# Kernel tuning notes

Measured on AMD Instinct MI355X. Metric: run time of the kernel, lower is better.

The kernel has to match this reference:

```python
import jax, jax.numpy as jnp
import numpy as np

N_P, N_D, N_S = 100000, 1000, 5000      # patients, drugs, diseases
C, H, L = 64, 4, 2                       # hidden, heads, layers
DH = C // H                              # head dim
IN_P, IN_D, IN_S = 64, 128, 64           # raw feature dims per node type
E_PD, E_DP, E_DS, E_PS = 300000, 300000, 100000, 100000
EPS = 1e-16


def setup_inputs() -> dict:
    key = jax.random.key(0)
    ks = jax.random.split(key, 20)

    def lin(k, fin, fout, prefix=()):
        return jax.random.normal(k, prefix + (fin, fout), jnp.float32) / np.sqrt(fin).astype(np.float32)

    def edges(k, e, n_src, n_dst):
        k1, k2 = jax.random.split(k)
        return jnp.stack([jax.random.randint(k1, (e,), 0, n_src),
                          jax.random.randint(k2, (e,), 0, n_dst)]).astype(jnp.int32)

    inp = {}
    inp['x_p'] = jax.random.normal(ks[0], (N_P, IN_P), jnp.float32)
    inp['x_d'] = jax.random.normal(ks[1], (N_D, IN_D), jnp.float32)
    inp['x_s'] = jax.random.normal(ks[2], (N_S, IN_S), jnp.float32)
    inp['Win_p'] = lin(ks[3], IN_P, C); inp['bin_p'] = jnp.zeros((C,), jnp.float32)
    inp['Win_d'] = lin(ks[4], IN_D, C); inp['bin_d'] = jnp.zeros((C,), jnp.float32)
    inp['Win_s'] = lin(ks[5], IN_S, C); inp['bin_s'] = jnp.zeros((C,), jnp.float32)
    inp['Wk'] = lin(ks[6], C, C, (L, 3)); inp['bk'] = jnp.zeros((L, 3, C), jnp.float32)
    inp['Wq'] = lin(ks[7], C, C, (L, 3)); inp['bq'] = jnp.zeros((L, 3, C), jnp.float32)
    inp['Wv'] = lin(ks[8], C, C, (L, 3)); inp['bv'] = jnp.zeros((L, 3, C), jnp.float32)
    inp['Wa'] = lin(ks[9], C, C, (L, 3)); inp['ba'] = jnp.zeros((L, 3, C), jnp.float32)
    inp['a_rel'] = jax.random.normal(ks[10], (L, 4, H, DH, DH), jnp.float32) / np.sqrt(DH).astype(np.float32)
    inp['m_rel'] = jax.random.normal(ks[11], (L, 4, H, DH, DH), jnp.float32) / np.sqrt(DH).astype(np.float32)
    inp['p_rel'] = jnp.ones((L, 4, H), jnp.float32)   # PyG inits rel prior to ones
    inp['skip'] = jnp.ones((L, 3), jnp.float32)       # PyG inits skip gate to ones
    inp['ei_pd'] = edges(ks[12], E_PD, N_P, N_D)  # patient -takes-> drug
    inp['ei_dp'] = edges(ks[13], E_DP, N_D, N_P)  # drug -taken_by-> patient
    inp['ei_ds'] = edges(ks[14], E_DS, N_D, N_S)  # drug -treats-> disease
    inp['ei_ps'] = edges(ks[15], E_PS, N_P, N_S)  # patient -has-> disease
    return inp


def _hgt(x_p, x_d, x_s, Win_p, bin_p, Win_d, bin_d, Win_s, bin_s,
         Wk, bk, Wq, bq, Wv, bv, Wa, ba, a_rel, m_rel, p_rel, skip,
         ei_pd, ei_dp, ei_ds, ei_ps):
    Ns = (N_P, N_D, N_S)
    # per-node-type input projection (lin_dict)
    xs = [x_p @ Win_p + bin_p, x_d @ Win_d + bin_d, x_s @ Win_s + bin_s]
    # (src_type, dst_type, edge_index) for each relation
    edge_defs = [(0, 1, ei_pd), (1, 0, ei_dp), (1, 2, ei_ds), (0, 2, ei_ps)]
    inv_sqrt_d = np.float32(1.0 / np.sqrt(DH))

    for l in range(L):  # HGTConv layers
        k_t = [(xs[t] @ Wk[l, t] + bk[l, t]).reshape(Ns[t], H, DH) for t in range(3)]
        q_t = [(xs[t] @ Wq[l, t] + bq[l, t]).reshape(Ns[t], H, DH) for t in range(3)]
        v_t = [(xs[t] @ Wv[l, t] + bv[l, t]).reshape(Ns[t], H, DH) for t in range(3)]
        out = [jnp.zeros((Ns[t], H, DH), xs[t].dtype) for t in range(3)]
        for r, (st, dt, ei) in enumerate(edge_defs):
            src, dst = ei[0], ei[1]
            # relation-specific head-wise transforms of K and V
            k_rel = jnp.einsum('nhd,hde->nhe', k_t[st], a_rel[l, r])
            v_rel = jnp.einsum('nhd,hde->nhe', v_t[st], m_rel[l, r])
            # attention logits per edge, per head: [E, H]
            alpha = (q_t[dt][dst] * k_rel[src]).sum(-1) * (p_rel[l, r] * inv_sqrt_d)
            # segment softmax over incoming edges of each dst node (per relation)
            mx = jax.ops.segment_max(alpha, dst, num_segments=Ns[dt])
            a = jnp.exp(alpha - jax.lax.stop_gradient(mx)[dst])
            den = jax.ops.segment_sum(a, dst, num_segments=Ns[dt])
            a = a / (den[dst] + EPS)
            # attention-weighted scatter-add of messages, grouped by 'sum'
            out[dt] = out[dt] + jax.ops.segment_sum(v_rel[src] * a[:, :, None], dst, num_segments=Ns[dt])
        new_xs = []
        for t in range(3):
            o = jax.nn.gelu(out[t].reshape(Ns[t], C), approximate=False) @ Wa[l, t] + ba[l, t]
            s = jax.nn.sigmoid(skip[l, t])  # learned skip gate (in == out channels)
            new_xs.append(s * o + (1.0 - s) * xs[t])
        xs = new_xs
    # concatenate node-type outputs along node axis: [N_P+N_D+N_S, C]
    return jnp.concatenate(xs, axis=0)


def reference(x_p, x_d, x_s, Win_p, bin_p, Win_d, bin_d, Win_s, bin_s,
              Wk, bk, Wq, bq, Wv, bv, Wa, ba, a_rel, m_rel, p_rel, skip,
              ei_pd, ei_dp, ei_ds, ei_ps):
    return _hgt(x_p, x_d, x_s, Win_p, bin_p, Win_d, bin_d, Win_s, bin_s,
                Wk, bk, Wq, bq, Wv, bv, Wa, ba, a_rel, m_rel, p_rel, skip,
                ei_pd, ei_dp, ei_ds, ei_ps)
```

## Files before the change

### kernel.cpp

```cpp
#include <hip/hip_runtime.h>
#include <cmath>

typedef unsigned short ush;
typedef __attribute__((ext_vector_type(8))) short short8;
typedef __attribute__((ext_vector_type(4))) float floatx4;

static constexpr int N_P = 100000, N_D = 1000, N_S = 5000, NT = N_P + N_D + N_S;
static constexpr int NC = 111000;
static constexpr int E_TOT = 800000;

static constexpr int NB0 = 128, NB2 = 64, NB3 = 64;
static constexpr int CH0 = (300000 + NB0 - 1) / NB0;
static constexpr int CH2 = (100000 + NB2 - 1) / NB2;
static constexpr int HB0_OFF = 0;
static constexpr int HB2_OFF = NB0 * 1000;
static constexpr int HB3_OFF = HB2_OFF + NB2 * 5000;
static constexpr int NCH0 = NB0 / 16, NCH2 = NB2 / 16;
static constexpr int CS0_OFF = 0;
static constexpr int CS2_OFF = NCH0 * 1000;
static constexpr int CS3_OFF = CS2_OFF + NCH2 * 5000;
static constexpr int NHIST = NB0 + NB2 + NB3;
static constexpr int NBLK_R1 = (300000 + 255) / 256;
static constexpr int NZB = (100000 + 255) / 256;

__device__ __forceinline__ float b2f(ush b) { return __uint_as_float(((unsigned)b) << 16); }
__device__ __forceinline__ ush f2b(float f) {
    unsigned u = __float_as_uint(f);
    return (ush)((u + 0x7FFFu + ((u >> 16) & 1u)) >> 16);
}

static constexpr size_t OFF_WINP = 0;
static constexpr size_t OFF_BINP = 4096;
static constexpr size_t OFF_WIND = 4160;
static constexpr size_t OFF_BIND = 12352;
static constexpr size_t OFF_WINS = 12416;
static constexpr size_t OFF_BINS = 16512;
static constexpr size_t OFF_WK = 16576;
static constexpr size_t OFF_BK = 41152;
static constexpr size_t OFF_WQ = 41536;
static constexpr size_t OFF_BQ = 66112;
static constexpr size_t OFF_WV = 66496;
static constexpr size_t OFF_BV = 91072;
static constexpr size_t OFF_WA = 91456;
static constexpr size_t OFF_BA = 116032;
static constexpr size_t OFF_AREL = 116416;
static constexpr size_t OFF_MREL = 124608;
static constexpr size_t OFF_PREL = 132800;
static constexpr size_t OFF_SKIP = 132832;
static constexpr size_t CW_TOTAL = 132838;
static constexpr int NCONVB = (int)((CW_TOTAL + 255) / 256);
static constexpr int NSCB = (NC + 1 + 255) / 256;

static constexpr size_t TWINP = 0;
static constexpr size_t TWIND = 4096;
static constexpr size_t TWINS = 12288;
static constexpr size_t TWQO = 16384;
static constexpr size_t TWAO = 40960;
static constexpr size_t TW_TOTAL = 65536;
static constexpr int NTWB = (int)(TW_TOTAL / 256);

struct ConvArgs {
    const void* src[18];
    long cum[19];
    int fl[18];
};

struct CsrB {
    const int* ei[3];
    const int* ei1;
};

__device__ __forceinline__ void hist_geom(int b, const CsrB& c, int& r, const int*& ei, int& E,
                                          int& ndst, int& e0, int& e1, int& hb) {
    if (b < NB0) {
        r = 0; ei = c.ei[0]; E = 300000; ndst = 1000;
        e0 = b * CH0; hb = HB0_OFF + b * 1000;
    } else if (b < NB0 + NB2) {
        r = 1; ei = c.ei[1]; E = 100000; ndst = 5000;
        e0 = (b - NB0) * CH2; hb = HB2_OFF + (b - NB0) * 5000;
    } else {
        r = 2; ei = c.ei[2]; E = 100000; ndst = 5000;
        e0 = (b - NB0 - NB2) * CH2; hb = HB3_OFF + (b - NB0 - NB2) * 5000;
    }
    e1 = min(E, e0 + ((r == 0) ? CH0 : CH2));
}

__device__ __forceinline__ bool cs_geom(int g, int& idx0, int& step) {
    if (g >= 48000) return false;
    if (g < 8000) {
        int c = g / 1000, d = g % 1000;
        idx0 = HB0_OFF + c * 16 * 1000 + d; step = 1000;
    } else if (g < 28000) {
        int gg = g - 8000, c = gg / 5000, d = gg % 5000;
        idx0 = HB2_OFF + c * 16 * 5000 + d; step = 5000;
    } else {
        int gg = g - 28000, c = gg / 5000, d = gg % 5000;
        idx0 = HB3_OFF + c * 16 * 5000 + d; step = 5000;
    }
    return true;
}

__global__ __launch_bounds__(256) void k1_kernel(ConvArgs a, ush* __restrict__ dst,
                                                 ush* __restrict__ tw,
                                                 int* __restrict__ cnt_r1, CsrB c,
                                                 int* __restrict__ HB) {
    const int b = blockIdx.x;
    if (b < NCONVB) {
        long g = (long)b * 256 + threadIdx.x;
        if (g >= (long)CW_TOTAL) return;
        int t = 0;
        while (g >= a.cum[t + 1]) t++;
        long i = g - a.cum[t];
        float v = a.fl[t] ? ((const float*)a.src[t])[i] : b2f(((const ush*)a.src[t])[i]);
        dst[g] = f2b(v);
    } else if (b < NCONVB + NZB) {
        int g = (b - NCONVB) * 256 + threadIdx.x;
        if (g < 100000) cnt_r1[g] = 0;
    } else if (b < NCONVB + NZB + NHIST) {
        __shared__ int h[5000];
        int r, E, ndst, e0, e1, hb;
        const int* ei;
        hist_geom(b - NCONVB - NZB, c, r, ei, E, ndst, e0, e1, hb);
        for (int d = threadIdx.x; d < ndst; d += 256) h[d] = 0;
        __syncthreads();
        for (int e = e0 + threadIdx.x; e < e1; e += 256) atomicAdd(&h[ei[E + e]], 1);
        __syncthreads();
        for (int d = threadIdx.x; d < ndst; d += 256) HB[hb + d] = h[d];
    } else {
        int g = (b - NCONVB - NZB - NHIST) * 256 + threadIdx.x;
        const void* src; int fl; long ibase; int e;
        if (g < 4096) { src = a.src[0]; fl = a.fl[0]; e = g; ibase = 0; }
        else if (g < 12288) { src = a.src[2]; fl = a.fl[2]; e = g - 4096; ibase = 0; }
        else if (g < 16384) { src = a.src[4]; fl = a.fl[4]; e = g - 12288; ibase = 0; }
        else if (g < 40960) { int ee = g - 16384; src = a.src[8]; fl = a.fl[8];
                              e = ee & 4095; ibase = (long)(ee >> 12) * 4096; }
        else { int ee = g - 40960; src = a.src[12]; fl = a.fl[12];
               e = ee & 4095; ibase = (long)(ee >> 12) * 4096; }
        int f = e >> 9, l = (e >> 3) & 63, j = e & 7;
        int s = f >> 2, cc = f & 3;
        long in = ibase + (long)(32 * s + ((l >> 4) << 3) + j) * 64 + 16 * cc + (l & 15);
        float v = fl ? ((const float*)src)[in] : b2f(((const ush*)src)[in]);
        tw[g] = f2b(v);
    }
}

template <int K>
__device__ __forceinline__ void stage_A(short* sA, const ush* __restrict__ X, int M, int row0) {
    for (int cid = threadIdx.x; cid < 64 * K / 8; cid += 256) {
        int r = cid / (K / 8), c0 = (cid % (K / 8)) * 8;
        int row = row0 + r;
        short8 v = {0, 0, 0, 0, 0, 0, 0, 0};
        if (row < M) v = *(const short8*)(const void*)(X + (size_t)row * K + c0);
        *(short8*)(&sA[r * (K + 8) + c0]) = v;
    }
}

template <int K>
__device__ __forceinline__ void stage_A_raw(short* sA, const void* __restrict__ X, int f,
                                            int M, int row0) {
    for (int cid = threadIdx.x; cid < 64 * K / 8; cid += 256) {
        int r = cid / (K / 8), c0 = (cid % (K / 8)) * 8;
        int row = row0 + r;
        short8 v = {0, 0, 0, 0, 0, 0, 0, 0};
        if (row < M) {
            if (f) {
                const floatx4* fp = (const floatx4*)((const float*)X + (size_t)row * K + c0);
                floatx4 f0 = fp[0], f1 = fp[1];
#pragma unroll
                for (int j = 0; j < 4; j++) v[j] = (short)f2b(f0[j]);
#pragma unroll
                for (int j = 0; j < 4; j++) v[4 + j] = (short)f2b(f1[j]);
            } else {
                v = *(const short8*)(const void*)((const ush*)X + (size_t)row * K + c0);
            }
        }
        *(short8*)(&sA[r * (K + 8) + c0]) = v;
    }
}

template <int K>
__device__ __forceinline__ void gemm_direct64(short* sA, const ush* __restrict__ WF,
                                              const ush* __restrict__ Bb,
                                              ush* __restrict__ Y, int M, int row0) {
    __syncthreads();
    const int tid = threadIdx.x;
    const int w = tid >> 6, l = tid & 63;
    floatx4 acc[4];
#pragma unroll
    for (int c = 0; c < 4; c++) {
        float bv = b2f(Bb[16 * c + (l & 15)]);
        acc[c] = (floatx4){bv, bv, bv, bv};
    }
#pragma unroll
    for (int s = 0; s < K / 32; s++) {
        short8 a = *(const short8*)(&sA[(16 * w + (l & 15)) * (K + 8) + 32 * s + ((l >> 4) << 3)]);
#pragma unroll
        for (int c = 0; c < 4; c++) {
            short8 b = *(const short8*)(const void*)(WF + ((size_t)(s * 4 + c) * 64 + l) * 8);
            acc[c] = __builtin_amdgcn_mfma_f32_16x16x32_bf16(a, b, acc[c], 0, 0, 0);
        }
    }
    __syncthreads();
#pragma unroll
    for (int c = 0; c < 4; c++)
#pragma unroll
        for (int r = 0; r < 4; r++)
            sA[(16 * w + ((l >> 4) << 2) + r) * 72 + 16 * c + (l & 15)] = (short)f2b(acc[c][r]);
    __syncthreads();
    for (int u = tid; u < 512; u += 256) {
        int r = u >> 3, c0 = (u & 7) * 8;
        int row = row0 + r;
        if (row < M)
            *(short8*)(Y + (size_t)row * 64 + c0) = *(const short8*)(&sA[r * 72 + c0]);
    }
}

template <int NG>
__device__ __forceinline__ void gemm_wideD(short* sA,
                                           const ush* __restrict__ Wq,
                                           const ush* __restrict__ Bq, ush* __restrict__ Yq,
                                           const ush* __restrict__ WeA,
                                           ush* __restrict__ YAk, ush* __restrict__ YAv,
                                           const ush* __restrict__ WeB,
                                           ush* __restrict__ YBk, ush* __restrict__ YBv,
                                           int M, int row0) {
    __syncthreads();
    const int tid = threadIdx.x;
    const int w = tid >> 6, l = tid & 63;
    floatx4 acc[NG];
#pragma unroll
    for (int c = 0; c < NG; c++) {
        float bv;
        if (c < 4) bv = b2f(Bq[16 * c + (l & 15)]);
        else if (c < 12) bv = b2f(WeA[8192 + 16 * (c - 4) + (l & 15)]);
        else bv = b2f(WeB[8192 + 16 * (c - 12) + (l & 15)]);
        acc[c] = (floatx4){bv, bv, bv, bv};
    }
#pragma unroll
    for (int s = 0; s < 2; s++) {
        short8 a = *(const short8*)(&sA[(16 * w + (l & 15)) * 72 + 32 * s + ((l >> 4) << 3)]);
#pragma unroll
        for (int c = 0; c < NG; c++) {
            const ush* bp;
            if (c < 4) bp = Wq + ((size_t)(s * 4 + c) * 64 + l) * 8;
            else if (c < 12) bp = WeA + ((size_t)(s * 8 + (c - 4)) * 64 + l) * 8;
            else bp = WeB + ((size_t)(s * 8 + (c - 12)) * 64 + l) * 8;
            short8 b = *(const short8*)(const void*)bp;
            acc[c] = __builtin_amdgcn_mfma_f32_16x16x32_bf16(a, b, acc[c], 0, 0, 0);
        }
    }
    ush* dst[5] = {Yq, YAk, YAv, YBk, YBv};
#pragma unroll
    for (int cg = 0; cg < NG / 4; cg++) {
        __syncthreads();
#pragma unroll
        for (int c2 = 0; c2 < 4; c2++)
#pragma unroll
            for (int r = 0; r < 4; r++)
                sA[(16 * w + ((l >> 4) << 2) + r) * 72 + 16 * c2 + (l & 15)] =
                    (short)f2b(acc[cg * 4 + c2][r]);
        __syncthreads();
        ush* Y = dst[cg];
        for (int u = tid; u < 512; u += 256) {
            int r = u >> 3, c0 = (u & 7) * 8;
            int row = row0 + r;
            if (row < M)
                *(short8*)(Y + (size_t)row * 64 + c0) = *(const short8*)(&sA[r * 72 + c0]);
        }
    }
}

struct K2Args {
    const void* raw[3];
    int f[3];
    const ush* W[3];
    const ush* Bb[3];
    ush* X;
    const int* HB;
    int* CS;
    int* cnt;
    const int* ei1;
};

__global__ __launch_bounds__(256) void k2_kernel(K2Args a) {
    extern __shared__ short smem[];
    const int b = blockIdx.x;
    if (b < 1658) {
        short* sA = smem;
        if (b < 1563) {
            stage_A_raw<64>(sA, a.raw[0], a.f[0], N_P, b * 64);
            gemm_direct64<64>(sA, a.W[0], a.Bb[0], a.X, N_P, b * 64);
        } else if (b < 1579) {
            stage_A_raw<128>(sA, a.raw[1], a.f[1], N_D, (b - 1563) * 64);
            gemm_direct64<128>(sA, a.W[1], a.Bb[1], a.X + (size_t)N_P * 64, N_D,
                               (b - 1563) * 64);
        } else {
            stage_A_raw<64>(sA, a.raw[2], a.f[2], N_S, (b - 1579) * 64);
            gemm_direct64<64>(sA, a.W[2], a.Bb[2], a.X + (size_t)(N_P + N_D) * 64, N_S,
                              (b - 1579) * 64);
        }
    } else if (b < 1701) {
        int d = (b - 1658) * 256 + threadIdx.x;
        if (d >= 11000) return;
        int ld_, nch, base, step, cs0, csstep, roff;
        if (d < 1000) { ld_ = d; nch = NCH0; base = HB0_OFF + ld_; step = 1000;
                        cs0 = CS0_OFF + ld_; csstep = 1000; roff = 0; }
        else if (d < 6000) { ld_ = d - 1000; nch = NCH2; base = HB2_OFF + ld_; step = 5000;
                             cs0 = CS2_OFF + ld_; csstep = 5000; roff = 101000; }
        else { ld_ = d - 6000; nch = NCH2; base = HB3_OFF + ld_; step = 5000;
               cs0 = CS3_OFF + ld_; csstep = 5000; roff = 106000; }
        int run = 0;
        for (int cc = 0; cc < nch; cc++) {
            int s = 0;
#pragma unroll
            for (int bb = 0; bb < 16; bb++) s += a.HB[base + (cc * 16 + bb) * step];
            a.CS[cs0 + cc * csstep] = run;
            run += s;
        }
        a.cnt[roff + ld_] = run;
    } else {
        int g = (b - 1701) * 256 + threadIdx.x;
        if (g < 300000) atomicAdd(&a.cnt[1000 + a.ei1[300000 + g]], 1);
    }
}

__global__ __launch_bounds__(256) void k3_kernel(const int* __restrict__ cnt,
                                                 int* __restrict__ tmp,
                                                 int* __restrict__ part,
                                                 const ush* __restrict__ CW,
                                                 ush* __restrict__ weff) {
    const int b = blockIdx.x;
    if (b < 109) {
        __shared__ int ls[256];
        const int t = threadIdx.x;
        const int base = b * 1024 + t * 4;
        int v[4];
#pragma unroll
        for (int j = 0; j < 4; j++) v[j] = (base + j < NC) ? cnt[base + j] : 0;
        int tsum = v[0] + v[1] + v[2] + v[3];
        ls[t] = tsum;
        __syncthreads();
        for (int off = 1; off < 256; off <<= 1) {
            int y = (t >= off) ? ls[t - off] : 0;
            __syncthreads();
            ls[t] += y;
            __syncthreads();
        }
        int run = ls[t] - tsum;
#pragma unroll
        for (int j = 0; j < 4; j++) {
            if (base + j < NC) tmp[base + j] = run;
            run += v[j];
        }
        if (t == 255) part[b] = ls[255];
    } else {
        const int eb = b - 109;
        const int l = eb >> 2, r = eb & 3;
        const int st_of[4] = {0, 1, 1, 0};
        const int st = st_of[r];
        ush* out = weff + (size_t)eb * 8320;
        for (int idx = threadIdx.x; idx < 8320; idx += 256) {
            int k, n;
            if (idx < 8192) {
                int f = idx >> 9, ll = (idx >> 3) & 63, j = idx & 7;
                int s = f >> 3, c = f & 7;
                k = 32 * s + ((ll >> 4) << 3) + j;
                n = 16 * c + (ll & 15);
            } else { k = -1; n = idx - 8192; }
            int kv = n >= 64;
            int jj = n & 63, h = jj >> 4, e = jj & 15;
            const ush* W = CW + (kv ? OFF_WV : OFF_WK) + (size_t)(l * 3 + st) * 4096;
            const ush* B = CW + (kv ? OFF_BV : OFF_BK) + (size_t)(l * 3 + st) * 64;
            const ush* R = CW + (kv ? OFF_MREL : OFF_AREL) + (size_t)(l * 4 + r) * 1024;
            float acc = 0.f;
            if (k >= 0) {
#pragma unroll
                for (int d = 0; d < 16; d++)
                    acc += b2f(W[k * 64 + h * 16 + d]) * b2f(R[h * 256 + d * 16 + e]);
            } else {
#pragma unroll
                for (int d = 0; d < 16; d++)
                    acc += b2f(B[h * 16 + d]) * b2f(R[h * 256 + d * 16 + e]);
            }
            out[idx] = f2b(acc);
        }
    }
}

__global__ __launch_bounds__(256) void k4_kernel(const int* __restrict__ tmp,
                                                 const int* __restrict__ part,
                                                 int* __restrict__ rowptr,
                                                 int* __restrict__ HB,
                                                 const int* __restrict__ CS,
                                                 int* __restrict__ fillpos) {
    const int b = blockIdx.x;
    if (b < NSCB) {
        __shared__ int ls[256];
        const int t = threadIdx.x;
        ls[t] = (t < 109) ? part[t] : 0;
        __syncthreads();
        for (int off = 1; off < 256; off <<= 1) {
            int y = (t >= off) ? ls[t - off] : 0;
            __syncthreads();
            ls[t] += y;
            __syncthreads();
        }
        int i = b * 256 + t;
        if (i <= NC)
            rowptr[i] = (i == NC) ? ls[255] : tmp[i] + ((i >> 10) ? ls[(i >> 10) - 1] : 0);
    } else if (b < NSCB + 188) {
        int g = (b - NSCB) * 256 + threadIdx.x;
        int idx0, step;
        if (!cs_geom(g, idx0, step)) return;
        int run = CS[g];
#pragma unroll
        for (int bb = 0; bb < 16; bb++) {
            int t2 = HB[idx0 + bb * step];
            HB[idx0 + bb * step] = run;
            run += t2;
        }
    } else {
        int g = (b - NSCB - 188) * 256 + threadIdx.x;
        if (g < 100000) fillpos[g] = 0;
    }
}

struct QKVArgs {
    const ush* X;
    ush* Q;
    ush* KVk[4];
    ush* KVv[4];
    const ush* Wq[3];
    const ush* Bq[3];
    const ush* We[4];
    CsrB cb;
    const int* HB;
    const int* rowptr;
    int* fillpos;
    int* col;
};

__global__ __launch_bounds__(256) void qkvfill_kernel(QKVArgs a) {
    extern __shared__ short smem[];
    const int b = blockIdx.x;
    if (b < 1658) {
        short* sA = smem;
        if (b < 1563) {
            stage_A<64>(sA, a.X, N_P, b * 64);
            gemm_wideD<20>(sA, a.Wq[0], a.Bq[0], a.Q,
                           a.We[0], a.KVk[0], a.KVv[0],
                           a.We[3], a.KVk[3], a.KVv[3], N_P, b * 64);
        } else if (b < 1579) {
            int lb = b - 1563;
            stage_A<64>(sA, a.X + (size_t)N_P * 64, N_D, lb * 64);
            gemm_wideD<20>(sA, a.Wq[1], a.Bq[1], a.Q + (size_t)N_P * 64,
                           a.We[1], a.KVk[1], a.KVv[1],
                           a.We[2], a.KVk[2], a.KVv[2], N_D, lb * 64);
        } else {
            int lb = b - 1579;
            stage_A<64>(sA, a.X + (size_t)(N_P + N_D) * 64, N_S, lb * 64);
            gemm_wideD<4>(sA, a.Wq[2], a.Bq[2], a.Q + (size_t)(N_P + N_D) * 64,
                          nullptr, nullptr, nullptr, nullptr, nullptr, nullptr,
                          N_S, lb * 64);
        }
    } else if (b < 1658 + NHIST) {
        int* h = (int*)smem;
        int r, E, ndst, e0, e1, hb;
        const int* ei;
        hist_geom(b - 1658, a.cb, r, ei, E, ndst, e0, e1, hb);
        const int roff = (r == 0) ? 0 : (r == 1) ? 101000 : 106000;
        for (int d = threadIdx.x; d < ndst; d += 256) h[d] = a.rowptr[roff + d] + a.HB[hb + d];
        __syncthreads();
        for (int e = e0 + threadIdx.x; e < e1; e += 256) {
            int d = ei[E + e];
            int slot = atomicAdd(&h[d], 1);
            a.col[slot] = ei[e];
        }
    } else {
        int g = (b - 1658 - NHIST) * 256 + threadIdx.x;
        if (g < 300000) {
            int gi = 1000 + a.cb.ei1[300000 + g];
            int slot = a.rowptr[gi] + atomicAdd(&a.fillpos[gi], 1);
            a.col[slot] = a.cb.ei1[g];
        }
    }
}

struct AggrArgs {
    const int* rowptr;
    const int* col;
    const ush* KVk[4];
    const ush* KVv[4];
    const ush* Q;
    const ush* prel;
    ush* OUT;
};

template <int LANES>
__device__ __forceinline__ void seg_attn(const AggrArgs& a, int rel, int g, int h, int lane,
                                         const float* qf, float* o) {
    const int s0 = a.rowptr[g], s1 = a.rowptr[g + 1];
    const ush* Kb = a.KVk[rel];
    const ush* Vb = a.KVv[rel];
    const float ps = b2f(a.prel[rel * 4 + h]) * 0.25f;
    float m = -1e30f, s = 0.f;
    float acc[16];
#pragma unroll
    for (int i = 0; i < 16; i++) acc[i] = 0.f;
    for (int j = s0 + lane; j < s1; j += LANES) {
        int src = a.col[j];
        const ush* kp = Kb + (size_t)src * 64 + h * 16;
        const ush* vp = Vb + (size_t)src * 64 + h * 16;
        short8 k0 = *(const short8*)(const void*)kp;
        short8 k1 = *(const short8*)(const void*)(kp + 8);
        short8 v0 = *(const short8*)(const void*)vp;
        short8 v1 = *(const short8*)(const void*)(vp + 8);
        float dot = 0.f;
#pragma unroll
        for (int i = 0; i < 8; i++) dot += qf[i] * b2f((ush)k0[i]);
#pragma unroll
        for (int i = 0; i < 8; i++) dot += qf[8 + i] * b2f((ush)k1[i]);
        float aa = dot * ps;
        float nm = fmaxf(m, aa);
        float e0 = __expf(m - nm), e1 = __expf(aa - nm);
        s = s * e0 + e1;
#pragma unroll
        for (int i = 0; i < 8; i++) acc[i] = acc[i] * e0 + e1 * b2f((ush)v0[i]);
#pragma unroll
        for (int i = 0; i < 8; i++) acc[8 + i] = acc[8 + i] * e0 + e1 * b2f((ush)v1[i]);
        m = nm;
    }
#pragma unroll
    for (int wd = LANES >> 1; wd >= 1; wd >>= 1) {
        float mo = __shfl_xor(m, wd);
        float so = __shfl_xor(s, wd);
        float nm = fmaxf(m, mo);
        float e0 = __expf(m - nm), e1 = __expf(mo - nm);
        s = s * e0 + so * e1;
#pragma unroll
        for (int i = 0; i < 16; i++) {
            float ao = __shfl_xor(acc[i], wd);
            acc[i] = acc[i] * e0 + ao * e1;
        }
        m = nm;
    }
    float inv = 1.f / (s + 1e-16f);
#pragma unroll
    for (int i = 0; i < 16; i++) o[i] += acc[i] * inv;
}

template <int LANES>
__device__ __forceinline__ void job_run(const AggrArgs& a, int wid, int nd, int rel, int roff,
                                        size_t xoff, int rel2, int roff2) {
    const int lane = wid % LANES;
    const int grp = wid / LANES;
    const int d = grp >> 2, h = grp & 3;
    if (d >= nd) return;
    const ush* qp = a.Q + xoff + (size_t)d * 64 + h * 16;
    short8 q0 = *(const short8*)(const void*)qp;
    short8 q1 = *(const short8*)(const void*)(qp + 8);
    float qf[16];
#pragma unroll
    for (int i = 0; i < 8; i++) { qf[i] = b2f((ush)q0[i]); qf[8 + i] = b2f((ush)q1[i]); }
    float o[16];
#pragma unroll
    for (int i = 0; i < 16; i++) o[i] = 0.f;
    seg_attn<LANES>(a, rel, roff + d, h, lane, qf, o);
    if (rel2 >= 0) seg_attn<LANES>(a, rel2, roff2 + d, h, lane, qf, o);
    if (lane == 0) {
        ush* op = a.OUT + xoff + (size_t)d * 64 + h * 16;
        short8 w0, w1;
#pragma unroll
        for (int i = 0; i < 8; i++) {
            float va = o[i];
            w0[i] = (short)f2b(0.5f * va * (1.0f + erff(va * 0.70710678118654752f)));
            float vb = o[8 + i];
            w1[i] = (short)f2b(0.5f * vb * (1.0f + erff(vb * 0.70710678118654752f)));
        }
        *(short8*)(op) = w0;
        *(short8*)(op + 8) = w1;
    }
}

__global__ __launch_bounds__(256) void aggr_kernel(AggrArgs a) {
    const int b = blockIdx.x, t = threadIdx.x;
    if (b < 250) {
        job_run<16>(a, b * 256 + t, N_D, 0, 0, (size_t)N_P * 64, -1, 0);
    } else if (b < 563) {
        job_run<4>(a, (b - 250) * 256 + t, N_S, 2, 101000, (size_t)(N_P + N_D) * 64, 3, 106000);
    } else {
        job_run<2>(a, (b - 563) * 256 + t, N_P, 1, 1000, 0, -1, 0);
    }
}

struct EpiArgs {
    const ush* O;
    ush* X;
    const ush* W[3];
    const ush* Bb[3];
    const ush* skipv;
    void* fout;
    int foutf;
    int last;
};

__global__ __launch_bounds__(256) void epi_kernel(EpiArgs a) {
    const int b = blockIdx.x;
    int t, lb, M;
    size_t noff;
    if (b < 1563) { t = 0; lb = b; M = N_P; noff = 0; }
    else if (b < 1579) { t = 1; lb = b - 1563; M = N_D; noff = (size_t)N_P; }
    else { t = 2; lb = b - 1579; M = N_S; noff = (size_t)(N_P + N_D); }
    const ush* O = a.O + noff * 64;
    ush* X = a.X + noff * 64;
    const ush* WF = a.W[t];
    __shared__ short sA[64 * 72];
    const int tid = threadIdx.x;
    const int row0 = lb * 64;
    for (int cid = tid; cid < 512; cid += 256) {
        int r = cid >> 3, c0 = (cid & 7) * 8;
        int row = row0 + r;
        short8 sv = {0, 0, 0, 0, 0, 0, 0, 0};
        if (row < M) sv = *(const short8*)(const void*)(O + (size_t)row * 64 + c0);
        *(short8*)(&sA[r * 72 + c0]) = sv;
    }
    __syncthreads();
    const float sg = 1.f / (1.f + expf(-b2f(a.skipv[t])));
    const int w = tid >> 6, l = tid & 63;
    floatx4 acc[4];
#pragma unroll
    for (int c = 0; c < 4; c++) {
        float bv = b2f(a.Bb[t][16 * c + (l & 15)]);
        acc[c] = (floatx4){bv, bv, bv, bv};
    }
#pragma unroll
    for (int s = 0; s < 2; s++) {
        short8 av = *(const short8*)(&sA[(16 * w + (l & 15)) * 72 + 32 * s + ((l >> 4) << 3)]);
#pragma unroll
        for (int c = 0; c < 4; c++) {
            short8 bv = *(const short8*)(const void*)(WF + ((size_t)(s * 4 + c) * 64 + l) * 8);
            acc[c] = __builtin_amdgcn_mfma_f32_16x16x32_bf16(av, bv, acc[c], 0, 0, 0);
        }
    }
    float* sOf = (float*)sA;
#pragma unroll
    for (int ch = 0; ch < 2; ch++) {
        __syncthreads();
        if ((w >> 1) == ch) {
#pragma unroll
            for (int c = 0; c < 4; c++)
#pragma unroll
                for (int r = 0; r < 4; r++)
                    sOf[(16 * (w & 1) + ((l >> 4) << 2) + r) * 68 + 16 * c + (l & 15)] =
                        acc[c][r];
        }
        __syncthreads();
        {
            int r = tid >> 3, c0 = (tid & 7) * 8;
            int row = row0 + ch * 32 + r;
            if (row < M) {
                floatx4 f0 = *(const floatx4*)(&sOf[r * 68 + c0]);
                floatx4 f1 = *(const floatx4*)(&sOf[r * 68 + c0 + 4]);
                short8 xv = *(const short8*)(const void*)(X + (size_t)row * 64 + c0);
                float vo[8];
#pragma unroll
                for (int j = 0; j < 4; j++) vo[j] = sg * f0[j] + (1.f - sg) * b2f((ush)xv[j]);
#pragma unroll
                for (int j = 0; j < 4; j++)
                    vo[4 + j] = sg * f1[j] + (1.f - sg) * b2f((ush)xv[4 + j]);
                if (!a.last) {
                    short8 ov;
#pragma unroll
                    for (int j = 0; j < 8; j++) ov[j] = (short)f2b(vo[j]);
                    *(short8*)(X + (size_t)row * 64 + c0) = ov;
                } else {
                    size_t goff = (noff + row) * 64 + c0;
                    if (a.foutf) {
                        floatx4 o0, o1;
#pragma unroll
                        for (int j = 0; j < 4; j++) { o0[j] = vo[j]; o1[j] = vo[4 + j]; }
                        *(floatx4*)((float*)a.fout + goff) = o0;
                        *(floatx4*)((float*)a.fout + goff + 4) = o1;
                    } else {
                        short8 ov;
#pragma unroll
                        for (int j = 0; j < 8; j++) ov[j] = (short)f2b(vo[j]);
                        *(short8*)((ush*)a.fout + goff) = ov;
                    }
                }
            }
        }
    }
}

extern "C" void kernel_launch(void* const* d_in, const int* in_sizes, int n_in,
                              void* d_out, int out_size, void* d_ws, size_t ws_size,
                              hipStream_t stream) {
    char* w = (char*)d_ws;
    w += 64;
    ush* CW = (ush*)w;      w += ((CW_TOTAL * 2 + 63) / 64) * 64;
    ush* WEFFB = (ush*)w;   w += ((size_t)8 * 8320 * 2 + 63) / 64 * 64;
    ush* TW = (ush*)w;      w += (size_t)TW_TOTAL * 2;
    ush* X = (ush*)w;       w += (size_t)NT * 64 * 2;
    ush* Q = (ush*)w;       w += (size_t)NT * 64 * 2;
    ush* KV0 = (ush*)w;     w += (size_t)N_P * 128 * 2;
    ush* KV1 = (ush*)w;     w += (size_t)N_D * 128 * 2;
    ush* KV2 = (ush*)w;     w += (size_t)N_D * 128 * 2;
    ush* KV3 = (ush*)w;     w += (size_t)N_P * 128 * 2;
    ush* OUT = (ush*)w;     w += (size_t)NT * 64 * 4;
    int* CNT = (int*)w;     w += (size_t)NC * 4;
    int* TMP = (int*)w;     w += (size_t)NC * 4;
    int* PART = (int*)w;    w += 512;
    int* ROWPTR = (int*)w;  w += (size_t)(NC + 1) * 4;
    int* COL = (int*)w;     w += (size_t)E_TOT * 4;
    int* HB = (int*)OUT;
    int* CS = (int*)OUT + 800000;

    static const long sz[18] = {4096, 64, 8192, 64, 4096, 64, 24576, 384, 24576, 384,
                                24576, 384, 24576, 384, 8192, 8192, 32, 6};
    ConvArgs ca;
    long cum = 0;
    for (int t = 0; t < 18; t++) {
        ca.src[t] = d_in[3 + t];
        ca.cum[t] = cum;
        ca.fl[t] = (in_sizes[3 + t] != (int)(sz[t] * 2)) ? 1 : 0;
        cum += sz[t];
    }
    ca.cum[18] = cum;

    CsrB cb;
    cb.ei[0] = (const int*)d_in[21];
    cb.ei[1] = (const int*)d_in[23];
    cb.ei[2] = (const int*)d_in[24];
    cb.ei1 = (const int*)d_in[22];

    k1_kernel<<<NCONVB + NZB + NHIST + NTWB, 256, 0, stream>>>(ca, CW, TW, CNT + 1000, cb, HB);

    K2Args k2;
    k2.raw[0] = d_in[0]; k2.f[0] = (in_sizes[0] != N_P * 64 * 2) ? 1 : 0;
    k2.raw[1] = d_in[1]; k2.f[1] = (in_sizes[1] != N_D * 128 * 2) ? 1 : 0;
    k2.raw[2] = d_in[2]; k2.f[2] = (in_sizes[2] != N_S * 64 * 2) ? 1 : 0;
    k2.W[0] = TW + TWINP; k2.Bb[0] = CW + OFF_BINP;
    k2.W[1] = TW + TWIND; k2.Bb[1] = CW + OFF_BIND;
    k2.W[2] = TW + TWINS; k2.Bb[2] = CW + OFF_BINS;
    k2.X = X;
    k2.HB = HB; k2.CS = CS; k2.cnt = CNT; k2.ei1 = cb.ei1;
    k2_kernel<<<1701 + NBLK_R1, 256, 17408, stream>>>(k2);

    k3_kernel<<<109 + 8, 256, 0, stream>>>(CNT, TMP, PART, CW, WEFFB);

    k4_kernel<<<NSCB + 188 + NZB, 256, 0, stream>>>(TMP, PART, ROWPTR, HB, CS, CNT + 1000);

    ush* KVr[4] = {KV0, KV1, KV2, KV3};
    const size_t nsr[4] = {(size_t)N_P, (size_t)N_D, (size_t)N_D, (size_t)N_P};
    const int foutf = (out_size != NT * 64 * 2) ? 1 : 0;

    for (int l = 0; l < 2; l++) {
        QKVArgs qk;
        qk.X = X;
        qk.Q = Q;
        for (int r = 0; r < 4; r++) {
            qk.KVk[r] = KVr[r];
            qk.KVv[r] = KVr[r] + nsr[r] * 64;
            qk.We[r] = WEFFB + (size_t)(l * 4 + r) * 8320;
        }
        for (int t = 0; t < 3; t++) {
            qk.Wq[t] = TW + TWQO + (size_t)(l * 3 + t) * 4096;
            qk.Bq[t] = CW + OFF_BQ + (l * 3 + t) * 64;
        }
        qk.cb = cb;
        qk.HB = HB;
        qk.rowptr = ROWPTR;
        qk.fillpos = CNT;
        qk.col = COL;
        const int qgrid = (l == 0) ? (1658 + NHIST + NBLK_R1) : 1658;
        const int qlds = (l == 0) ? 20000 : 9216;
        qkvfill_kernel<<<qgrid, 256, qlds, stream>>>(qk);

        AggrArgs aa;
        aa.rowptr = ROWPTR;
        aa.col = COL;
        for (int r = 0; r < 4; r++) {
            aa.KVk[r] = KVr[r];
            aa.KVv[r] = KVr[r] + nsr[r] * 64;
        }
        aa.Q = Q;
        aa.prel = CW + OFF_PREL + l * 16;
        aa.OUT = OUT;
        aggr_kernel<<<3688, 256, 0, stream>>>(aa);

        EpiArgs ea;
        ea.O = OUT;
        ea.X = X;
        for (int t = 0; t < 3; t++) {
            ea.W[t] = TW + TWAO + (size_t)(l * 3 + t) * 4096;
            ea.Bb[t] = CW + OFF_BA + (l * 3 + t) * 64;
        }
        ea.skipv = CW + OFF_SKIP + l * 3;
        ea.fout = d_out;
        ea.foutf = foutf;
        ea.last = (l == 1) ? 1 : 0;
        epi_kernel<<<1658, 256, 0, stream>>>(ea);
    }
}
```

Before: 401.8 us.

## Stage GEMM weight fragments in LDS and split qkv from CSR fill kernel

Each GEMM block now copies its weight fragments into shared memory once and reads the MFMA B operands from LDS, instead of every wave loading them from global memory. This applies to the input projection, the fused Q/K/V projection and the epilogue. The combined qkv+fill kernel is split into a dedicated qkv kernel and a separate fill kernel launched only for layer 0. The extra LDS (up to about 50KB for qkv) can lower occupancy, and splitting the kernel removes the overlap the fused launch gave between the fill work and the GEMMs.

Result: faster. 384.0 us (-4.4%).

```diff
diff --git a/kernel.cpp b/kernel.cpp
--- a/kernel.cpp
+++ b/kernel.cpp
@@ -179,11 +179,14 @@
 }
 
 template <int K>
-__device__ __forceinline__ void gemm_direct64(short* sA, const ush* __restrict__ WF,
-                                              const ush* __restrict__ Bb,
-                                              ush* __restrict__ Y, int M, int row0) {
+__device__ __forceinline__ void gemm_core64(const short* sA, short* sB,
+                                            const ush* __restrict__ W, const ush* __restrict__ Bb,
+                                            ush* __restrict__ Y, int M, int row0) {
+    constexpr int NF = (K / 32) * 4;
+    const int tid = threadIdx.x;
+    for (int u = tid; u < NF * 64; u += 256)
+        *(short8*)(&sB[u * 8]) = *(const short8*)(const void*)(W + (size_t)u * 8);
     __syncthreads();
-    const int tid = threadIdx.x;
     const int w = tid >> 6, l = tid & 63;
     floatx4 acc[4];
 #pragma unroll
@@ -196,7 +199,7 @@
         short8 a = *(const short8*)(&sA[(16 * w + (l & 15)) * (K + 8) + 32 * s + ((l >> 4) << 3)]);
 #pragma unroll
         for (int c = 0; c < 4; c++) {
-            short8 b = *(const short8*)(const void*)(WF + ((size_t)(s * 4 + c) * 64 + l) * 8);
+            short8 b = *(const short8*)(&sB[(s * 4 + c) * 512 + l * 8]);
             acc[c] = __builtin_amdgcn_mfma_f32_16x16x32_bf16(a, b, acc[c], 0, 0, 0);
         }
     }
@@ -205,27 +208,38 @@
     for (int c = 0; c < 4; c++)
 #pragma unroll
         for (int r = 0; r < 4; r++)
-            sA[(16 * w + ((l >> 4) << 2) + r) * 72 + 16 * c + (l & 15)] = (short)f2b(acc[c][r]);
+            sB[(16 * w + ((l >> 4) << 2) + r) * 72 + 16 * c + (l & 15)] =
+                (short)f2b(acc[c][r]);
     __syncthreads();
     for (int u = tid; u < 512; u += 256) {
         int r = u >> 3, c0 = (u & 7) * 8;
         int row = row0 + r;
         if (row < M)
-            *(short8*)(Y + (size_t)row * 64 + c0) = *(const short8*)(&sA[r * 72 + c0]);
+            *(short8*)(Y + (size_t)row * 64 + c0) = *(const short8*)(&sB[r * 72 + c0]);
     }
 }
 
 template <int NG>
-__device__ __forceinline__ void gemm_wideD(short* sA,
-                                           const ush* __restrict__ Wq,
-                                           const ush* __restrict__ Bq, ush* __restrict__ Yq,
-                                           const ush* __restrict__ WeA,
-                                           ush* __restrict__ YAk, ush* __restrict__ YAv,
-                                           const ush* __restrict__ WeB,
-                                           ush* __restrict__ YBk, ush* __restrict__ YBv,
-                                           int M, int row0) {
+__device__ __forceinline__ void gemm_wide(const short* sA, short* sB,
+                                          const ush* __restrict__ Wq, const ush* __restrict__ Bq,
+                                          ush* __restrict__ Yq,
+                                          const ush* __restrict__ WeA,
+                                          ush* __restrict__ YAk, ush* __restrict__ YAv,
+                                          const ush* __restrict__ WeB,
+                                          ush* __restrict__ YBk, ush* __restrict__ YBv,
+                                          int M, int row0) {
+    constexpr int NF = 2 * NG;
+    const int tid = threadIdx.x;
+    for (int u = tid; u < NF * 64; u += 256) {
+        int f = u >> 6, k = u & 63;
+        int s = f / NG, c = f % NG;
+        const ush* src;
+        if (c < 4) src = Wq + (size_t)(s * 4 + c) * 512;
+        else if (c < 12) src = WeA + (size_t)(s * 8 + (c - 4)) * 512;
+        else src = WeB + (size_t)(s * 8 + (c - 12)) * 512;
+        *(short8*)(&sB[f * 512 + k * 8]) = *(const short8*)(const void*)(src + k * 8);
+    }
     __syncthreads();
-    const int tid = threadIdx.x;
     const int w = tid >> 6, l = tid & 63;
     floatx4 acc[NG];
 #pragma unroll
@@ -241,11 +255,7 @@
         short8 a = *(const short8*)(&sA[(16 * w + (l & 15)) * 72 + 32 * s + ((l >> 4) << 3)]);
 #pragma unroll
         for (int c = 0; c < NG; c++) {
-            const ush* bp;
-            if (c < 4) bp = Wq + ((size_t)(s * 4 + c) * 64 + l) * 8;
-            else if (c < 12) bp = WeA + ((size_t)(s * 8 + (c - 4)) * 64 + l) * 8;
-            else bp = WeB + ((size_t)(s * 8 + (c - 12)) * 64 + l) * 8;
-            short8 b = *(const short8*)(const void*)bp;
+            short8 b = *(const short8*)(&sB[(s * NG + c) * 512 + l * 8]);
             acc[c] = __builtin_amdgcn_mfma_f32_16x16x32_bf16(a, b, acc[c], 0, 0, 0);
         }
     }
@@ -257,7 +267,7 @@
         for (int c2 = 0; c2 < 4; c2++)
 #pragma unroll
             for (int r = 0; r < 4; r++)
-                sA[(16 * w + ((l >> 4) << 2) + r) * 72 + 16 * c2 + (l & 15)] =
+                sB[(16 * w + ((l >> 4) << 2) + r) * 72 + 16 * c2 + (l & 15)] =
                     (short)f2b(acc[cg * 4 + c2][r]);
         __syncthreads();
         ush* Y = dst[cg];
@@ -265,7 +275,7 @@
             int r = u >> 3, c0 = (u & 7) * 8;
             int row = row0 + r;
             if (row < M)
-                *(short8*)(Y + (size_t)row * 64 + c0) = *(const short8*)(&sA[r * 72 + c0]);
+                *(short8*)(Y + (size_t)row * 64 + c0) = *(const short8*)(&sB[r * 72 + c0]);
         }
     }
 }
@@ -286,18 +296,20 @@
     extern __shared__ short smem[];
     const int b = blockIdx.x;
     if (b < 1658) {
-        short* sA = smem;
         if (b < 1563) {
+            short* sA = smem; short* sB = smem + 64 * 72;
             stage_A_raw<64>(sA, a.raw[0], a.f[0], N_P, b * 64);
-            gemm_direct64<64>(sA, a.W[0], a.Bb[0], a.X, N_P, b * 64);
+            gemm_core64<64>(sA, sB, a.W[0], a.Bb[0], a.X, N_P, b * 64);
         } else if (b < 1579) {
+            short* sA = smem; short* sB = smem + 64 * 136;
             stage_A_raw<128>(sA, a.raw[1], a.f[1], N_D, (b - 1563) * 64);
-            gemm_direct64<128>(sA, a.W[1], a.Bb[1], a.X + (size_t)N_P * 64, N_D,
-                               (b - 1563) * 64);
+            gemm_core64<128>(sA, sB, a.W[1], a.Bb[1], a.X + (size_t)N_P * 64, N_D,
+                             (b - 1563) * 64);
         } else {
+            short* sA = smem; short* sB = smem + 64 * 72;
             stage_A_raw<64>(sA, a.raw[2], a.f[2], N_S, (b - 1579) * 64);
-            gemm_direct64<64>(sA, a.W[2], a.Bb[2], a.X + (size_t)(N_P + N_D) * 64, N_S,
-                              (b - 1579) * 64);
+            gemm_core64<64>(sA, sB, a.W[2], a.Bb[2], a.X + (size_t)(N_P + N_D) * 64, N_S,
+                            (b - 1579) * 64);
         }
     } else if (b < 1701) {
         int d = (b - 1658) * 256 + threadIdx.x;
@@ -433,6 +445,34 @@
     const ush* Wq[3];
     const ush* Bq[3];
     const ush* We[4];
+};
+
+__global__ __launch_bounds__(256) void qkv_kernel(QKVArgs a) {
+    extern __shared__ short smem[];
+    const int b = blockIdx.x;
+    short* sA = smem;
+    short* sB = smem + 64 * 72;
+    if (b < 1563) {
+        stage_A<64>(sA, a.X, N_P, b * 64);
+        gemm_wide<20>(sA, sB, a.Wq[0], a.Bq[0], a.Q,
+                      a.We[0], a.KVk[0], a.KVv[0],
+                      a.We[3], a.KVk[3], a.KVv[3], N_P, b * 64);
+    } else if (b < 1579) {
+        int lb = b - 1563;
+        stage_A<64>(sA, a.X + (size_t)N_P * 64, N_D, lb * 64);
+        gemm_wide<20>(sA, sB, a.Wq[1], a.Bq[1], a.Q + (size_t)N_P * 64,
+                      a.We[1], a.KVk[1], a.KVv[1],
+                      a.We[2], a.KVk[2], a.KVv[2], N_D, lb * 64);
+    } else {
+        int lb = b - 1579;
+        stage_A<64>(sA, a.X + (size_t)(N_P + N_D) * 64, N_S, lb * 64);
+        gemm_wide<4>(sA, sB, a.Wq[2], a.Bq[2], a.Q + (size_t)(N_P + N_D) * 64,
+                     nullptr, nullptr, nullptr, nullptr, nullptr, nullptr,
+                     N_S, lb * 64);
+    }
+}
+
+struct FillArgs {
     CsrB cb;
     const int* HB;
     const int* rowptr;
@@ -440,34 +480,14 @@
     int* col;
 };
 
-__global__ __launch_bounds__(256) void qkvfill_kernel(QKVArgs a) {
+__global__ __launch_bounds__(256) void fill_kernel(FillArgs a) {
     extern __shared__ short smem[];
     const int b = blockIdx.x;
-    if (b < 1658) {
-        short* sA = smem;
-        if (b < 1563) {
-            stage_A<64>(sA, a.X, N_P, b * 64);
-            gemm_wideD<20>(sA, a.Wq[0], a.Bq[0], a.Q,
-                           a.We[0], a.KVk[0], a.KVv[0],
-                           a.We[3], a.KVk[3], a.KVv[3], N_P, b * 64);
-        } else if (b < 1579) {
-            int lb = b - 1563;
-            stage_A<64>(sA, a.X + (size_t)N_P * 64, N_D, lb * 64);
-            gemm_wideD<20>(sA, a.Wq[1], a.Bq[1], a.Q + (size_t)N_P * 64,
-                           a.We[1], a.KVk[1], a.KVv[1],
-                           a.We[2], a.KVk[2], a.KVv[2], N_D, lb * 64);
-        } else {
-            int lb = b - 1579;
-            stage_A<64>(sA, a.X + (size_t)(N_P + N_D) * 64, N_S, lb * 64);
-            gemm_wideD<4>(sA, a.Wq[2], a.Bq[2], a.Q + (size_t)(N_P + N_D) * 64,
-                          nullptr, nullptr, nullptr, nullptr, nullptr, nullptr,
-                          N_S, lb * 64);
-        }
-    } else if (b < 1658 + NHIST) {
+    if (b < NHIST) {
         int* h = (int*)smem;
         int r, E, ndst, e0, e1, hb;
         const int* ei;
-        hist_geom(b - 1658, a.cb, r, ei, E, ndst, e0, e1, hb);
+        hist_geom(b, a.cb, r, ei, E, ndst, e0, e1, hb);
         const int roff = (r == 0) ? 0 : (r == 1) ? 101000 : 106000;
         for (int d = threadIdx.x; d < ndst; d += 256) h[d] = a.rowptr[roff + d] + a.HB[hb + d];
         __syncthreads();
@@ -477,7 +497,7 @@
             a.col[slot] = ei[e];
         }
     } else {
-        int g = (b - 1658 - NHIST) * 256 + threadIdx.x;
+        int g = (b - NHIST) * 256 + threadIdx.x;
         if (g < 300000) {
             int gi = 1000 + a.cb.ei1[300000 + g];
             int slot = a.rowptr[gi] + atomicAdd(&a.fillpos[gi], 1);
@@ -615,6 +635,7 @@
     ush* X = a.X + noff * 64;
     const ush* WF = a.W[t];
     __shared__ short sA[64 * 72];
+    __shared__ short sB[8 * 512];
     const int tid = threadIdx.x;
     const int row0 = lb * 64;
     for (int cid = tid; cid < 512; cid += 256) {
@@ -624,6 +645,8 @@
         if (row < M) sv = *(const short8*)(const void*)(O + (size_t)row * 64 + c0);
         *(short8*)(&sA[r * 72 + c0]) = sv;
     }
+    for (int u = tid; u < 512; u += 256)
+        *(short8*)(&sB[u * 8]) = *(const short8*)(const void*)(WF + (size_t)u * 8);
     __syncthreads();
     const float sg = 1.f / (1.f + expf(-b2f(a.skipv[t])));
     const int w = tid >> 6, l = tid & 63;
@@ -638,7 +661,7 @@
         short8 av = *(const short8*)(&sA[(16 * w + (l & 15)) * 72 + 32 * s + ((l >> 4) << 3)]);
 #pragma unroll
         for (int c = 0; c < 4; c++) {
-            short8 bv = *(const short8*)(const void*)(WF + ((size_t)(s * 4 + c) * 64 + l) * 8);
+            short8 bv = *(const short8*)(&sB[(s * 4 + c) * 512 + l * 8]);
             acc[c] = __builtin_amdgcn_mfma_f32_16x16x32_bf16(av, bv, acc[c], 0, 0, 0);
         }
     }
@@ -745,7 +768,7 @@
     k2.W[2] = TW + TWINS; k2.Bb[2] = CW + OFF_BINS;
     k2.X = X;
     k2.HB = HB; k2.CS = CS; k2.cnt = CNT; k2.ei1 = cb.ei1;
-    k2_kernel<<<1701 + NBLK_R1, 256, 17408, stream>>>(k2);
+    k2_kernel<<<1701 + NBLK_R1, 256, 33792, stream>>>(k2);
 
     k3_kernel<<<109 + 8, 256, 0, stream>>>(CNT, TMP, PART, CW, WEFFB);
 
@@ -768,14 +791,17 @@
             qk.Wq[t] = TW + TWQO + (size_t)(l * 3 + t) * 4096;
             qk.Bq[t] = CW + OFF_BQ + (l * 3 + t) * 64;
         }
-        qk.cb = cb;
-        qk.HB = HB;
-        qk.rowptr = ROWPTR;
-        qk.fillpos = CNT;
-        qk.col = COL;
-        const int qgrid = (l == 0) ? (1658 + NHIST + NBLK_R1) : 1658;
-        const int qlds = (l == 0) ? 20000 : 9216;
-        qkvfill_kernel<<<qgrid, 256, qlds, stream>>>(qk);
+        qkv_kernel<<<1658, 256, 50176, stream>>>(qk);
+
+        if (l == 0) {
+            FillArgs fa;
+            fa.cb = cb;
+            fa.HB = HB;
+            fa.rowptr = ROWPTR;
+            fa.fillpos = CNT;
+            fa.col = COL;
+            fill_kernel<<<NHIST + NBLK_R1, 256, 20000, stream>>>(fa);
+        }
 
         AggrArgs aa;
         aa.rowptr = ROWPTR;
```
